# Kernel optimization log

Measured on AMD Instinct MI355X. Metric: run time of the kernel, lower is better.

Reference implementation:

```python
import jax, jax.numpy as jnp
import numpy as np

N, E, IN, H, OUT, L, G = 50000, 800000, 128, 128, 64, 3, 64
NEG_SLOPE = 0.2


def setup_inputs() -> dict:
    key = jax.random.key(0)
    ks = jax.random.split(key, 10)
    x = jax.random.normal(ks[0], (N, IN), dtype=jnp.float32)
    edge_index = jax.random.randint(ks[1], (2, E), 0, N, dtype=jnp.int64)
    batch = jnp.sort(jax.random.randint(ks[2], (N,), 0, G, dtype=jnp.int64))
    s_in = 1.0 / np.sqrt(IN)
    s_h = 1.0 / np.sqrt(H)
    return {
        "x": x,
        "edge_index": edge_index,
        "batch": batch,
        "W0": jax.random.normal(ks[3], (IN, H), dtype=jnp.float32) * s_in,
        "b0": jnp.zeros((H,), dtype=jnp.float32),
        "Wl": jax.random.normal(ks[4], (L, H, H), dtype=jnp.float32) * s_h,
        "a_src": jax.random.normal(ks[5], (L, H), dtype=jnp.float32) * s_h,
        "a_dst": jax.random.normal(ks[6], (L, H), dtype=jnp.float32) * s_h,
        "bl": jnp.zeros((L, H), dtype=jnp.float32),
        "Wf": jax.random.normal(ks[7], (H, OUT), dtype=jnp.float32) * s_h,
        "bf": jnp.zeros((OUT,), dtype=jnp.float32),
    }


def _gat_layer(h, src, dst, n_nodes, W, a_s, a_d, b):
    # GATConv, heads=1: h' = W h; e_ij = leaky_relu(a_s.h'_j + a_d.h'_i)
    hp = h @ W  # [N, H]
    alpha_s = hp @ a_s  # [N]
    alpha_d = hp @ a_d  # [N]
    e = jax.nn.leaky_relu(alpha_s[src] + alpha_d[dst], NEG_SLOPE)  # [E+N]
    # segment softmax over incoming edges of each destination node
    m = jax.ops.segment_max(e, dst, num_segments=n_nodes)
    ex = jnp.exp(e - m[dst])
    denom = jax.ops.segment_sum(ex, dst, num_segments=n_nodes)
    alpha = ex / denom[dst]  # [E+N]
    out = jax.ops.segment_sum(hp[src] * alpha[:, None], dst, num_segments=n_nodes)
    return out + b


def reference(x, edge_index, batch, W0, b0, Wl, a_src, a_dst, bl, Wf, bf):
    n_nodes = x.shape[0]
    loops = jnp.arange(n_nodes, dtype=edge_index.dtype)
    src = jnp.concatenate([edge_index[0], loops])  # add_self_loops=True
    dst = jnp.concatenate([edge_index[1], loops])
    h = x @ W0 + b0  # initial Linear
    n_layers = Wl.shape[0]
    for l in range(n_layers):
        h = _gat_layer(h, src, dst, n_nodes, Wl[l], a_src[l], a_dst[l], bl[l])
        if l < n_layers - 1:
            h = jax.nn.relu(h)  # BasicGNN: act between layers, none after last
    pooled = jax.ops.segment_sum(h, batch, num_segments=G)  # global_add_pool
    return (pooled @ Wf + bf).squeeze()
```

## Files before the change

### kernel.cpp

```cpp
#include <hip/hip_runtime.h>
#include <hip/hip_bf16.h>
#include <math.h>

#define HF 128
#define GCOUNT 64
#define OUTF 64
#define NEG 0.2f
#define CH 2048
#define BCAP 8192

typedef unsigned short u16;
typedef unsigned int   u32;
typedef unsigned char  u8;
typedef short bf16x8 __attribute__((ext_vector_type(8)));
typedef float f32x4  __attribute__((ext_vector_type(4)));
typedef float f32x2  __attribute__((ext_vector_type(2)));

__device__ __forceinline__ u16 f2b(float f) {
    u32 u = __builtin_bit_cast(u32, f);
    u32 r = (u + 0x7FFFu + ((u >> 16) & 1u)) >> 16;
    return (u16)r;
}

__device__ __forceinline__ u8 f2q(float f) {
    return (u8)(__builtin_amdgcn_cvt_pk_fp8_f32(f, f, 0, false) & 0xFF);
}

__global__ void k_pack_init(const float* __restrict__ W0, const float* __restrict__ Wl,
                            u16* __restrict__ P, int* bucketCur, float* pooled) {
    if (blockIdx.x < 32) {
        int m = blockIdx.x >> 3;
        int i = (blockIdx.x & 7) * 256 + threadIdx.x;
        const float* W = (m == 0) ? W0 : Wl + (size_t)(m - 1) * HF * HF;
        u16* Pm = P + (size_t)m * HF * HF;
        int lane = i & 63, kc = (i >> 6) & 3, t = i >> 8;
        int quad = lane >> 4, col = 16 * t + (lane & 15);
        #pragma unroll
        for (int j = 0; j < 8; ++j) {
            int k = kc * 32 + quad * 8 + j;
            Pm[(size_t)i * 8 + j] = f2b(W[k * HF + col]);
        }
    } else if (blockIdx.x == 32) {
        bucketCur[threadIdx.x] = threadIdx.x * BCAP;
    } else {
        pooled[(blockIdx.x - 33) * 256 + threadIdx.x] = 0.f;
    }
}


__device__ __forceinline__ void dev_bpart(int bx, const int* __restrict__ esrc,
                                          const int* __restrict__ edst,
                                          int* __restrict__ bucketCur,
                                          u32* __restrict__ epart, int ne, int ntot) {
    __shared__ int cnt[256];
    __shared__ int base[256];
    int tid = threadIdx.x;
    int t0 = bx * CH, t1 = min(t0 + CH, ntot);
    cnt[tid] = 0;
    __syncthreads();
    int sreg[8], dreg[8];
    #pragma unroll
    for (int it = 0; it < 8; ++it) {
        int t = t0 + tid + it * 256;
        int s = 0, d = -1;
        if (t < t1) {
            if (t < ne) { s = esrc[t]; d = edst[t]; }
            else        { s = t - ne; d = s; }
            atomicAdd(&cnt[d >> 8], 1);
        }
        sreg[it] = s; dreg[it] = d;
    }
    __syncthreads();
    int c = cnt[tid];
    base[tid] = c ? atomicAdd(&bucketCur[tid], c) : 0;
    cnt[tid] = 0;
    __syncthreads();
    #pragma unroll
    for (int it = 0; it < 8; ++it) {
        int d = dreg[it];
        if (d >= 0) {
            int b = d >> 8;
            int pos = base[b] + atomicAdd(&cnt[b], 1);
            epart[pos] = ((u32)sreg[it] << 8) | (u32)(d & 255);
        }
    }
}

__device__ __forceinline__ void dev_bcsr(int bx, const u32* __restrict__ epart,
                                         const int* __restrict__ bucketCur,
                                         int* __restrict__ rowbeg,
                                         int* __restrict__ rowend,
                                         int* __restrict__ colidx, int n) {
    __shared__ int deg[256], offs[256], curs[256], s[256];
    int b = bx, tid = threadIdx.x;
    int e0 = b * BCAP, e1 = bucketCur[b];
    deg[tid] = 0;
    curs[tid] = 0;
    __syncthreads();
    for (int t = e0 + tid; t < e1; t += 256)
        atomicAdd(&deg[epart[t] & 255u], 1);
    __syncthreads();
    int v = deg[tid];
    s[tid] = v;
    __syncthreads();
    int acc = v;
    for (int off = 1; off < 256; off <<= 1) {
        int t = (tid >= off) ? s[tid - off] : 0;
        __syncthreads();
        acc += t;
        s[tid] = acc;
        __syncthreads();
    }
    int excl = acc - v;
    offs[tid] = excl;
    int node = (b << 8) + tid;
    if (node < n) {
        rowbeg[node] = e0 + excl;
        rowend[node] = e0 + excl + v;
    }
    __syncthreads();
    for (int t = e0 + tid; t < e1; t += 256) {
        u32 e = epart[t];
        int l = e & 255u;
        int pos = e0 + offs[l] + atomicAdd(&curs[l], 1);
        colidx[pos] = (int)(e >> 8);
    }
}

template<bool A32, bool Q8>
__device__ __forceinline__ void dev_gemm(int bx, const u16* __restrict__ Ab,
                                         const float* __restrict__ Af,
                                         const u16* __restrict__ Bp,
                                         const float* __restrict__ bias,
                                         const float* __restrict__ a_s,
                                         const float* __restrict__ a_d,
                                         float* __restrict__ as_,
                                         float* __restrict__ ad_,
                                         u16* __restrict__ C,
                                         u8* __restrict__ C8, int M) {
    int lane = threadIdx.x & 63;
    int wave = threadIdx.x >> 6;
    int quad = lane >> 4, l16 = lane & 15;
    int m0 = bx * 64 + wave * 16;
    int arow = m0 + l16;
    bool aval = arow < M;
    const bf16x8* Av = A32 ? nullptr : (const bf16x8*)(Ab + (size_t)arow * HF);
    const bf16x8* Bv = (const bf16x8*)Bp;
    f32x4 acc[8] = {};

    #pragma unroll
    for (int kc = 0; kc < 4; ++kc) {
        bf16x8 a = {};
        if (aval) {
            if constexpr (A32) {
                const float* ap = Af + (size_t)arow * HF + kc * 32 + quad * 8;
                float4 f0 = *(const float4*)ap;
                float4 f1 = *(const float4*)(ap + 4);
                a[0] = (short)f2b(f0.x); a[1] = (short)f2b(f0.y);
                a[2] = (short)f2b(f0.z); a[3] = (short)f2b(f0.w);
                a[4] = (short)f2b(f1.x); a[5] = (short)f2b(f1.y);
                a[6] = (short)f2b(f1.z); a[7] = (short)f2b(f1.w);
            } else {
                a = Av[kc * 4 + quad];
            }
        }
        #pragma unroll
        for (int t = 0; t < 8; ++t)
            acc[t] = __builtin_amdgcn_mfma_f32_16x16x32_bf16(a, Bv[t * 256 + kc * 64 + lane],
                                                             acc[t], 0, 0, 0);
    }

    int orow0 = m0 + quad * 4;
    #pragma unroll
    for (int t = 0; t < 8; ++t) {
        float b4 = bias ? bias[t * 16 + l16] : 0.f;
        #pragma unroll
        for (int r = 0; r < 4; ++r) {
            int orow = orow0 + r;
            if (orow < M) {
                float v = acc[t][r] + b4;
                if constexpr (Q8) C8[(size_t)orow * HF + t * 16 + l16] = f2q(v);
                else              C [(size_t)orow * HF + t * 16 + l16] = f2b(v);
            }
        }
    }

    if (as_) {
        float avs[8], avd[8];
        #pragma unroll
        for (int t = 0; t < 8; ++t) {
            avs[t] = a_s[t * 16 + l16];
            avd[t] = a_d[t * 16 + l16];
        }
        #pragma unroll
        for (int r = 0; r < 4; ++r) {
            float ps = 0.f, pd = 0.f;
            #pragma unroll
            for (int t = 0; t < 8; ++t) {
                ps = fmaf(acc[t][r], avs[t], ps);
                pd = fmaf(acc[t][r], avd[t], pd);
            }
            #pragma unroll
            for (int o = 1; o < 16; o <<= 1) {
                ps += __shfl_xor(ps, o);
                pd += __shfl_xor(pd, o);
            }
            int row = orow0 + r;
            if (l16 == 0 && row < M) { as_[row] = ps; ad_[row] = pd; }
        }
    }
}

__global__ __launch_bounds__(256) void k_gemm0_bpart(const float* __restrict__ x,
                                                     const u16* __restrict__ Wp,
                                                     const float* __restrict__ b0,
                                                     u16* __restrict__ hb, int M, int gemmb,
                                                     const int* __restrict__ esrc,
                                                     const int* __restrict__ edst,
                                                     int* __restrict__ bucketCur,
                                                     u32* __restrict__ epart, int ne, int ntot) {
    if ((int)blockIdx.x < gemmb)
        dev_gemm<true, false>(blockIdx.x, nullptr, x, Wp, b0,
                              nullptr, nullptr, nullptr, nullptr, hb, nullptr, M);
    else
        dev_bpart(blockIdx.x - gemmb, esrc, edst, bucketCur, epart, ne, ntot);
}

__global__ __launch_bounds__(256) void k_gemm1_bcsr(const u16* __restrict__ hb,
                                                    const u16* __restrict__ Bp,
                                                    const float* __restrict__ a_s,
                                                    const float* __restrict__ a_d,
                                                    float* __restrict__ as_,
                                                    float* __restrict__ ad_,
                                                    u8* __restrict__ hp8, int M, int gemmb,
                                                    const u32* __restrict__ epart,
                                                    const int* __restrict__ bucketCur,
                                                    int* __restrict__ rowbeg,
                                                    int* __restrict__ rowend,
                                                    int* __restrict__ colidx, int n) {
    if ((int)blockIdx.x < gemmb)
        dev_gemm<false, true>(blockIdx.x, hb, nullptr, Bp, nullptr,
                              a_s, a_d, as_, ad_, nullptr, hp8, M);
    else
        dev_bcsr(blockIdx.x - gemmb, epart, bucketCur, rowbeg, rowend, colidx, n);
}

__global__ __launch_bounds__(256) void k_gemm_layer(const u16* __restrict__ hb,
                                                    const u16* __restrict__ Bp,
                                                    const float* __restrict__ a_s,
                                                    const float* __restrict__ a_d,
                                                    float* __restrict__ as_,
                                                    float* __restrict__ ad_,
                                                    u8* __restrict__ hp8, int M) {
    dev_gemm<false, true>(blockIdx.x, hb, nullptr, Bp, nullptr,
                          a_s, a_d, as_, ad_, nullptr, hp8, M);
}

template<bool POOL>
__device__ __forceinline__ void dev_agg_item(int it, const int* __restrict__ rowbeg,
                                             const int* __restrict__ rowend,
                                             const int* __restrict__ colidx,
                                             const u8* __restrict__ hp8,
                                             const float* __restrict__ as_,
                                             const float* __restrict__ ad_,
                                             const float* __restrict__ bl,
                                             u16* __restrict__ hout,
                                             int n, int relu,
                                             const int* __restrict__ batch,
                                             float* __restrict__ pooled) {
    int wv = threadIdx.x >> 6;
    int node = it * 4 + wv;
    int lane = threadIdx.x & 63;
    bool valid = node < n;
    int beg = 0, end = 0;
    float adi = 0.f;
    if (valid) { beg = rowbeg[node]; end = rowend[node]; adi = ad_[node]; }
    int deg = end - beg;

    int  srcl = (lane < deg) ? colidx[beg + lane] : 0;
    float el = -1e30f;
    if (lane < deg) {
        float e = as_[srcl] + adi;
        el = e > 0.f ? e : NEG * e;
    }

    float m = el;
    for (int jj = beg + 64 + lane; jj < end; jj += 64) {
        float e = as_[colidx[jj]] + adi;
        e = e > 0.f ? e : NEG * e;
        m = fmaxf(m, e);
    }
    #pragma unroll
    for (int off = 32; off; off >>= 1) m = fmaxf(m, __shfl_xor(m, off));

    float ex = (lane < deg) ? __expf(el - m) : 0.f;
    float ssum = ex;
    for (int jj = beg + 64 + lane; jj < end; jj += 64) {
        float e = as_[colidx[jj]] + adi;
        e = e > 0.f ? e : NEG * e;
        ssum += __expf(e - m);
    }
    #pragma unroll
    for (int off = 32; off; off >>= 1) ssum += __shfl_xor(ssum, off);
    float wl = ex;

    int hl = lane & 31;
    int half = lane >> 5;
    float a0 = 0.f, a1 = 0.f, a2 = 0.f, a3 = 0.f;
    int cnt = deg < 64 ? deg : 64;
    int npair = (cnt + 1) >> 1;

    int p = 0;
    for (; p + 4 <= npair; p += 4) {
        #pragma unroll
        for (int i = 0; i < 4; ++i) {
            int e  = 2 * (p + i) + half;
            int ec = e < cnt ? e : cnt - 1;
            int   s = __shfl(srcl, ec);
            float w = (e < cnt) ? __shfl(wl, ec) : 0.f;
            u32 v = ((const u32*)(hp8 + (size_t)s * HF))[hl];
            f32x2 lo = __builtin_amdgcn_cvt_pk_f32_fp8((int)v, false);
            f32x2 hi = __builtin_amdgcn_cvt_pk_f32_fp8((int)v, true);
            a0 = fmaf(w, lo.x, a0); a1 = fmaf(w, lo.y, a1);
            a2 = fmaf(w, hi.x, a2); a3 = fmaf(w, hi.y, a3);
        }
    }
    for (; p < npair; ++p) {
        int e  = 2 * p + half;
        int ec = e < cnt ? e : cnt - 1;
        int   s = __shfl(srcl, ec);
        float w = (e < cnt) ? __shfl(wl, ec) : 0.f;
        u32 v = ((const u32*)(hp8 + (size_t)s * HF))[hl];
        f32x2 lo = __builtin_amdgcn_cvt_pk_f32_fp8((int)v, false);
        f32x2 hi = __builtin_amdgcn_cvt_pk_f32_fp8((int)v, true);
        a0 = fmaf(w, lo.x, a0); a1 = fmaf(w, lo.y, a1);
        a2 = fmaf(w, hi.x, a2); a3 = fmaf(w, hi.y, a3);
    }
    for (int jj = beg + 64; jj < end; ++jj) {
        int srcn = colidx[jj];
        float e = as_[srcn] + adi;
        e = e > 0.f ? e : NEG * e;
        float w = (half == 0) ? __expf(e - m) : 0.f;
        u32 v = ((const u32*)(hp8 + (size_t)srcn * HF))[hl];
        f32x2 lo = __builtin_amdgcn_cvt_pk_f32_fp8((int)v, false);
        f32x2 hi = __builtin_amdgcn_cvt_pk_f32_fp8((int)v, true);
        a0 = fmaf(w, lo.x, a0); a1 = fmaf(w, lo.y, a1);
        a2 = fmaf(w, hi.x, a2); a3 = fmaf(w, hi.y, a3);
    }

    a0 += __shfl_xor(a0, 32); a1 += __shfl_xor(a1, 32);
    a2 += __shfl_xor(a2, 32); a3 += __shfl_xor(a3, 32);

    if constexpr (!POOL) {
        if (half == 0 && valid) {
            float inv = 1.f / ssum;
            float4 bb = ((const float4*)bl)[hl];
            a0 = fmaf(a0, inv, bb.x); a1 = fmaf(a1, inv, bb.y);
            a2 = fmaf(a2, inv, bb.z); a3 = fmaf(a3, inv, bb.w);
            if (relu) {
                a0 = fmaxf(a0, 0.f); a1 = fmaxf(a1, 0.f);
                a2 = fmaxf(a2, 0.f); a3 = fmaxf(a3, 0.f);
            }
            uint2 o;
            o.x = ((u32)f2b(a1) << 16) | (u32)f2b(a0);
            o.y = ((u32)f2b(a3) << 16) | (u32)f2b(a2);
            ((uint2*)(hout + (size_t)node * HF))[hl] = o;
        }
    } else {
        __shared__ float ptile[4][HF];
        if (half == 0) {
            float o0 = 0.f, o1 = 0.f, o2 = 0.f, o3 = 0.f;
            if (valid) {
                float inv = 1.f / ssum;
                float4 bb = ((const float4*)bl)[hl];
                o0 = fmaf(a0, inv, bb.x); o1 = fmaf(a1, inv, bb.y);
                o2 = fmaf(a2, inv, bb.z); o3 = fmaf(a3, inv, bb.w);
            }
            ptile[wv][hl * 4 + 0] = o0; ptile[wv][hl * 4 + 1] = o1;
            ptile[wv][hl * 4 + 2] = o2; ptile[wv][hl * 4 + 3] = o3;
        }
        __syncthreads();
        int tid = threadIdx.x;
        if (tid < HF) {
            float acc = 0.f;
            int curb = -1;
            #pragma unroll
            for (int s2 = 0; s2 < 4; ++s2) {
                int nd = it * 4 + s2;
                if (nd < n) {
                    int b = batch[nd];
                    if (b != curb) {
                        if (curb >= 0) atomicAdd(&pooled[curb * HF + tid], acc);
                        curb = b;
                        acc = 0.f;
                    }
                    acc += ptile[s2][tid];
                }
            }
            if (curb >= 0) atomicAdd(&pooled[curb * HF + tid], acc);
        }
    }
}

__global__ __launch_bounds__(256) void k_agg(const int* __restrict__ rowbeg,
                                             const int* __restrict__ rowend,
                                             const int* __restrict__ colidx,
                                             const u8* __restrict__ hp8,
                                             const float* __restrict__ as_,
                                             const float* __restrict__ ad_,
                                             const float* __restrict__ bl,
                                             u16* __restrict__ hout,
                                             int n, int relu) {
    dev_agg_item<false>(blockIdx.x, rowbeg, rowend, colidx, hp8, as_, ad_, bl,
                        hout, n, relu, nullptr, nullptr);
}

__global__ __launch_bounds__(256) void k_agg_pool(const int* __restrict__ rowbeg,
                                                  const int* __restrict__ rowend,
                                                  const int* __restrict__ colidx,
                                                  const u8* __restrict__ hp8,
                                                  const float* __restrict__ as_,
                                                  const float* __restrict__ ad_,
                                                  const float* __restrict__ bl,
                                                  int n,
                                                  const int* __restrict__ batch,
                                                  float* __restrict__ pooled) {
    dev_agg_item<true>(blockIdx.x, rowbeg, rowend, colidx, hp8, as_, ad_, bl,
                       nullptr, n, 0, batch, pooled);
}

__global__ void k_final(const float* __restrict__ pooled, const float* __restrict__ Wf,
                        const float* __restrict__ bf, float* __restrict__ out) {
    int g = blockIdx.x, o = threadIdx.x;
    float acc = bf[o];
    #pragma unroll 8
    for (int k = 0; k < HF; ++k) acc = fmaf(pooled[g * HF + k], Wf[k * OUTF + o], acc);
    out[g * OUTF + o] = acc;
}

extern "C" void kernel_launch(void* const* d_in, const int* in_sizes, int n_in,
                              void* d_out, int out_size, void* d_ws, size_t ws_size,
                              hipStream_t stream) {
    const float* x      = (const float*)d_in[0];
    const int*   edge   = (const int*)d_in[1];
    const int*   batch  = (const int*)d_in[2];
    const float* W0     = (const float*)d_in[3];
    const float* b0     = (const float*)d_in[4];
    const float* Wl     = (const float*)d_in[5];
    const float* a_src  = (const float*)d_in[6];
    const float* a_dst  = (const float*)d_in[7];
    const float* bl     = (const float*)d_in[8];
    const float* Wf     = (const float*)d_in[9];
    const float* bf     = (const float*)d_in[10];
    float* out = (float*)d_out;

    const int N  = in_sizes[2];
    const int E  = in_sizes[1] / 2;
    const int Et = E + N;
    const int L  = 3;
    const int NB = (N + 255) >> 8;

    char* ws = (char*)d_ws;
    size_t off = 0;
    auto alloc = [&](size_t bytes) { char* p = ws + off; off += (bytes + 255) & ~(size_t)255; return p; };
    u16*   hb      = (u16*)alloc((size_t)N * HF * 2);
    u8*    hp8     = (u8*)alloc((size_t)N * HF);
    u16*   Wp      = (u16*)alloc((size_t)4 * HF * HF * 2);
    float* as_     = (float*)alloc((size_t)N * 4);
    float* ad_     = (float*)alloc((size_t)N * 4);
    int*   rowbeg  = (int*)alloc((size_t)N * 4);
    int*   rowend  = (int*)alloc((size_t)N * 4);
    int*   colidx  = (int*)alloc((size_t)NB * BCAP * 4);
    u32*   epart   = (u32*)alloc((size_t)NB * BCAP * 4);
    int*   bucketCur = (int*)alloc(256 * 4);
    float* pooled  = (float*)alloc((size_t)GCOUNT * HF * 4);
    (void)ws_size; (void)n_in; (void)out_size;

    const int wb4   = (N + 3) / 4;
    const int gemmb = (N + 63) / 64;
    const int partb = (Et + CH - 1) / CH;

    const int* esrc = edge;
    const int* edst = edge + E;

    k_pack_init<<<65, 256, 0, stream>>>(W0, Wl, Wp, bucketCur, pooled);

    k_gemm0_bpart<<<gemmb + partb, 256, 0, stream>>>(x, Wp, b0, hb, N, gemmb,
                                                     esrc, edst, bucketCur, epart, E, Et);

    k_gemm1_bcsr<<<gemmb + NB, 256, 0, stream>>>(hb, Wp + (size_t)1 * HF * HF,
                                                 a_src, a_dst, as_, ad_, hp8, N, gemmb,
                                                 epart, bucketCur, rowbeg, rowend, colidx, N);

    for (int l = 0; l < L; ++l) {
        if (l > 0)
            k_gemm_layer<<<gemmb, 256, 0, stream>>>(hb, Wp + (size_t)(l + 1) * HF * HF,
                                                    a_src + l * HF, a_dst + l * HF,
                                                    as_, ad_, hp8, N);
        if (l < L - 1)
            k_agg<<<wb4, 256, 0, stream>>>(rowbeg, rowend, colidx, hp8, as_, ad_,
                                           bl + l * HF, hb, N, 1);
        else
            k_agg_pool<<<wb4, 256, 0, stream>>>(rowbeg, rowend, colidx, hp8, as_, ad_,
                                                bl + l * HF, N, batch, pooled);
    }

    k_final<<<GCOUNT, OUTF, 0, stream>>>(pooled, Wf, bf, out);
}
```

Baseline: 266.3 us.

## Software-pipeline fp8 neighbor gathers with 16-lane rows and 8-byte loads

Restructures the aggregation gather so each node row is handled by 16 lanes doing 8-byte fp8 loads, with four edges in flight per group instead of two. Loads for the first edge group are issued before the softmax max/sum reductions, and the following groups are double-buffered so memory latency overlaps with compute. This is meant to hide gather latency and cut the number of load instructions. In exchange it uses more registers (8 accumulators plus 8 u64 buffers) and needs an extra cross-lane reduction step.

```diff
diff --git a/kernel.cpp b/kernel.cpp
--- a/kernel.cpp
+++ b/kernel.cpp
@@ -12,6 +12,7 @@
 typedef unsigned short u16;
 typedef unsigned int   u32;
 typedef unsigned char  u8;
+typedef unsigned long long u64;
 typedef short bf16x8 __attribute__((ext_vector_type(8)));
 typedef float f32x4  __attribute__((ext_vector_type(4)));
 typedef float f32x2  __attribute__((ext_vector_type(2)));
@@ -46,7 +47,6 @@
         pooled[(blockIdx.x - 33) * 256 + threadIdx.x] = 0.f;
     }
 }
-
 
 __device__ __forceinline__ void dev_bpart(int bx, const int* __restrict__ esrc,
                                           const int* __restrict__ edst,
@@ -256,6 +256,46 @@
                           a_s, a_d, as_, ad_, nullptr, hp8, M);
 }
 
+__device__ __forceinline__ void agg_fma(u64 q, float w, float (&acc)[8]) {
+    u32 lo = (u32)q, hi = (u32)(q >> 32);
+    f32x2 p0 = __builtin_amdgcn_cvt_pk_f32_fp8((int)lo, false);
+    f32x2 p1 = __builtin_amdgcn_cvt_pk_f32_fp8((int)lo, true);
+    f32x2 p2 = __builtin_amdgcn_cvt_pk_f32_fp8((int)hi, false);
+    f32x2 p3 = __builtin_amdgcn_cvt_pk_f32_fp8((int)hi, true);
+    acc[0] = fmaf(w, p0.x, acc[0]); acc[1] = fmaf(w, p0.y, acc[1]);
+    acc[2] = fmaf(w, p1.x, acc[2]); acc[3] = fmaf(w, p1.y, acc[3]);
+    acc[4] = fmaf(w, p2.x, acc[4]); acc[5] = fmaf(w, p2.y, acc[5]);
+    acc[6] = fmaf(w, p3.x, acc[6]); acc[7] = fmaf(w, p3.y, acc[7]);
+}
+
+#define AGG_ISSUE(g, q0, q1, q2, q3)                                             \
+    {                                                                            \
+        int e0_ = (g)*16 + 0*4 + sub, e1_ = (g)*16 + 1*4 + sub;                  \
+        int e2_ = (g)*16 + 2*4 + sub, e3_ = (g)*16 + 3*4 + sub;                  \
+        int s0_ = __shfl(srcl, min(e0_, ecmax));                                 \
+        int s1_ = __shfl(srcl, min(e1_, ecmax));                                 \
+        int s2_ = __shfl(srcl, min(e2_, ecmax));                                 \
+        int s3_ = __shfl(srcl, min(e3_, ecmax));                                 \
+        q0 = *(const u64*)(hp8 + (size_t)s0_ * HF + fo);                         \
+        q1 = *(const u64*)(hp8 + (size_t)s1_ * HF + fo);                         \
+        q2 = *(const u64*)(hp8 + (size_t)s2_ * HF + fo);                         \
+        q3 = *(const u64*)(hp8 + (size_t)s3_ * HF + fo);                         \
+    }
+
+#define AGG_CONSUME(g, q0, q1, q2, q3)                                           \
+    {                                                                            \
+        int e0_ = (g)*16 + 0*4 + sub, e1_ = (g)*16 + 1*4 + sub;                  \
+        int e2_ = (g)*16 + 2*4 + sub, e3_ = (g)*16 + 3*4 + sub;                  \
+        float w0_ = __shfl(wl, min(e0_, ecmax));                                 \
+        float w1_ = __shfl(wl, min(e1_, ecmax));                                 \
+        float w2_ = __shfl(wl, min(e2_, ecmax));                                 \
+        float w3_ = __shfl(wl, min(e3_, ecmax));                                 \
+        agg_fma(q0, (e0_ < cnt) ? w0_ : 0.f, acc);                               \
+        agg_fma(q1, (e1_ < cnt) ? w1_ : 0.f, acc);                               \
+        agg_fma(q2, (e2_ < cnt) ? w2_ : 0.f, acc);                               \
+        agg_fma(q3, (e3_ < cnt) ? w3_ : 0.f, acc);                               \
+    }
+
 template<bool POOL>
 __device__ __forceinline__ void dev_agg_item(int it, const int* __restrict__ rowbeg,
                                              const int* __restrict__ rowend,
@@ -271,19 +311,27 @@
     int wv = threadIdx.x >> 6;
     int node = it * 4 + wv;
     int lane = threadIdx.x & 63;
+    int sub = lane >> 4;
+    int fo  = (lane & 15) * 8;
     bool valid = node < n;
     int beg = 0, end = 0;
     float adi = 0.f;
     if (valid) { beg = rowbeg[node]; end = rowend[node]; adi = ad_[node]; }
     int deg = end - beg;
-
-    int  srcl = (lane < deg) ? colidx[beg + lane] : 0;
+    int cnt = deg < 64 ? deg : 64;
+    int ecmax = cnt > 1 ? cnt - 1 : 0;
+
+    int srcl = (lane < deg) ? colidx[beg + lane] : 0;
+
+    float acc[8] = {};
+    u64 qA0, qA1, qA2, qA3, qB0, qB1, qB2, qB3;
+    AGG_ISSUE(0, qA0, qA1, qA2, qA3);
+
     float el = -1e30f;
     if (lane < deg) {
         float e = as_[srcl] + adi;
         el = e > 0.f ? e : NEG * e;
     }
-
     float m = el;
     for (int jj = beg + 64 + lane; jj < end; jj += 64) {
         float e = as_[colidx[jj]] + adi;
@@ -304,85 +352,77 @@
     for (int off = 32; off; off >>= 1) ssum += __shfl_xor(ssum, off);
     float wl = ex;
 
-    int hl = lane & 31;
-    int half = lane >> 5;
-    float a0 = 0.f, a1 = 0.f, a2 = 0.f, a3 = 0.f;
-    int cnt = deg < 64 ? deg : 64;
-    int npair = (cnt + 1) >> 1;
-
-    int p = 0;
-    for (; p + 4 <= npair; p += 4) {
-        #pragma unroll
-        for (int i = 0; i < 4; ++i) {
-            int e  = 2 * (p + i) + half;
-            int ec = e < cnt ? e : cnt - 1;
-            int   s = __shfl(srcl, ec);
-            float w = (e < cnt) ? __shfl(wl, ec) : 0.f;
-            u32 v = ((const u32*)(hp8 + (size_t)s * HF))[hl];
-            f32x2 lo = __builtin_amdgcn_cvt_pk_f32_fp8((int)v, false);
-            f32x2 hi = __builtin_amdgcn_cvt_pk_f32_fp8((int)v, true);
-            a0 = fmaf(w, lo.x, a0); a1 = fmaf(w, lo.y, a1);
-            a2 = fmaf(w, hi.x, a2); a3 = fmaf(w, hi.y, a3);
-        }
-    }
-    for (; p < npair; ++p) {
-        int e  = 2 * p + half;
-        int ec = e < cnt ? e : cnt - 1;
-        int   s = __shfl(srcl, ec);
-        float w = (e < cnt) ? __shfl(wl, ec) : 0.f;
-        u32 v = ((const u32*)(hp8 + (size_t)s * HF))[hl];
-        f32x2 lo = __builtin_amdgcn_cvt_pk_f32_fp8((int)v, false);
-        f32x2 hi = __builtin_amdgcn_cvt_pk_f32_fp8((int)v, true);
-        a0 = fmaf(w, lo.x, a0); a1 = fmaf(w, lo.y, a1);
-        a2 = fmaf(w, hi.x, a2); a3 = fmaf(w, hi.y, a3);
-    }
-    for (int jj = beg + 64; jj < end; ++jj) {
-        int srcn = colidx[jj];
-        float e = as_[srcn] + adi;
-        e = e > 0.f ? e : NEG * e;
-        float w = (half == 0) ? __expf(e - m) : 0.f;
-        u32 v = ((const u32*)(hp8 + (size_t)srcn * HF))[hl];
-        f32x2 lo = __builtin_amdgcn_cvt_pk_f32_fp8((int)v, false);
-        f32x2 hi = __builtin_amdgcn_cvt_pk_f32_fp8((int)v, true);
-        a0 = fmaf(w, lo.x, a0); a1 = fmaf(w, lo.y, a1);
-        a2 = fmaf(w, hi.x, a2); a3 = fmaf(w, hi.y, a3);
-    }
-
-    a0 += __shfl_xor(a0, 32); a1 += __shfl_xor(a1, 32);
-    a2 += __shfl_xor(a2, 32); a3 += __shfl_xor(a3, 32);
+    bool g1 = cnt > 16, g2 = cnt > 32, g3 = cnt > 48;
+    if (g1) AGG_ISSUE(1, qB0, qB1, qB2, qB3);
+    AGG_CONSUME(0, qA0, qA1, qA2, qA3);
+    if (g1) {
+        if (g2) AGG_ISSUE(2, qA0, qA1, qA2, qA3);
+        AGG_CONSUME(1, qB0, qB1, qB2, qB3);
+        if (g2) {
+            if (g3) AGG_ISSUE(3, qB0, qB1, qB2, qB3);
+            AGG_CONSUME(2, qA0, qA1, qA2, qA3);
+            if (g3) AGG_CONSUME(3, qB0, qB1, qB2, qB3);
+        }
+    }
+
+    for (int jj = beg + 64; jj < end; jj += 4) {
+        int e = jj + sub;
+        bool v = e < end;
+        int s = colidx[v ? e : end - 1];
+        float w = 0.f;
+        if (v) {
+            float x = as_[s] + adi;
+            x = x > 0.f ? x : NEG * x;
+            w = __expf(x - m);
+        }
+        u64 q = *(const u64*)(hp8 + (size_t)s * HF + fo);
+        agg_fma(q, w, acc);
+    }
+
+    #pragma unroll
+    for (int k = 0; k < 8; ++k) {
+        acc[k] += __shfl_xor(acc[k], 16);
+        acc[k] += __shfl_xor(acc[k], 32);
+    }
 
     if constexpr (!POOL) {
-        if (half == 0 && valid) {
+        if (lane < 16 && valid) {
             float inv = 1.f / ssum;
-            float4 bb = ((const float4*)bl)[hl];
-            a0 = fmaf(a0, inv, bb.x); a1 = fmaf(a1, inv, bb.y);
-            a2 = fmaf(a2, inv, bb.z); a3 = fmaf(a3, inv, bb.w);
+            float4 bb0 = ((const float4*)bl)[lane * 2];
+            float4 bb1 = ((const float4*)bl)[lane * 2 + 1];
+            float o0 = fmaf(acc[0], inv, bb0.x), o1 = fmaf(acc[1], inv, bb0.y);
+            float o2 = fmaf(acc[2], inv, bb0.z), o3 = fmaf(acc[3], inv, bb0.w);
+            float o4 = fmaf(acc[4], inv, bb1.x), o5 = fmaf(acc[5], inv, bb1.y);
+            float o6 = fmaf(acc[6], inv, bb1.z), o7 = fmaf(acc[7], inv, bb1.w);
             if (relu) {
-                a0 = fmaxf(a0, 0.f); a1 = fmaxf(a1, 0.f);
-                a2 = fmaxf(a2, 0.f); a3 = fmaxf(a3, 0.f);
-            }
-            uint2 o;
-            o.x = ((u32)f2b(a1) << 16) | (u32)f2b(a0);
-            o.y = ((u32)f2b(a3) << 16) | (u32)f2b(a2);
-            ((uint2*)(hout + (size_t)node * HF))[hl] = o;
+                o0 = fmaxf(o0, 0.f); o1 = fmaxf(o1, 0.f);
+                o2 = fmaxf(o2, 0.f); o3 = fmaxf(o3, 0.f);
+                o4 = fmaxf(o4, 0.f); o5 = fmaxf(o5, 0.f);
+                o6 = fmaxf(o6, 0.f); o7 = fmaxf(o7, 0.f);
+            }
+            uint4 o;
+            o.x = ((u32)f2b(o1) << 16) | (u32)f2b(o0);
+            o.y = ((u32)f2b(o3) << 16) | (u32)f2b(o2);
+            o.z = ((u32)f2b(o5) << 16) | (u32)f2b(o4);
+            o.w = ((u32)f2b(o7) << 16) | (u32)f2b(o6);
+            ((uint4*)(hout + (size_t)node * HF))[lane] = o;
         }
     } else {
         __shared__ float ptile[4][HF];
-        if (half == 0) {
-            float o0 = 0.f, o1 = 0.f, o2 = 0.f, o3 = 0.f;
-            if (valid) {
-                float inv = 1.f / ssum;
-                float4 bb = ((const float4*)bl)[hl];
-                o0 = fmaf(a0, inv, bb.x); o1 = fmaf(a1, inv, bb.y);
-                o2 = fmaf(a2, inv, bb.z); o3 = fmaf(a3, inv, bb.w);
-            }
-            ptile[wv][hl * 4 + 0] = o0; ptile[wv][hl * 4 + 1] = o1;
-            ptile[wv][hl * 4 + 2] = o2; ptile[wv][hl * 4 + 3] = o3;
+        if (lane < 16) {
+            float inv = valid ? 1.f / ssum : 0.f;
+            float4 bb0 = ((const float4*)bl)[lane * 2];
+            float4 bb1 = ((const float4*)bl)[lane * 2 + 1];
+            #pragma unroll
+            for (int k = 0; k < 8; ++k) {
+                float b = (k < 4) ? ((const float*)&bb0)[k] : ((const float*)&bb1)[k - 4];
+                ptile[wv][lane * 8 + k] = valid ? fmaf(acc[k], inv, b) : 0.f;
+            }
         }
         __syncthreads();
         int tid = threadIdx.x;
         if (tid < HF) {
-            float acc = 0.f;
+            float a = 0.f;
             int curb = -1;
             #pragma unroll
             for (int s2 = 0; s2 < 4; ++s2) {
@@ -390,14 +430,14 @@
                 if (nd < n) {
                     int b = batch[nd];
                     if (b != curb) {
-                        if (curb >= 0) atomicAdd(&pooled[curb * HF + tid], acc);
+                        if (curb >= 0) atomicAdd(&pooled[curb * HF + tid], a);
                         curb = b;
-                        acc = 0.f;
+                        a = 0.f;
                     }
-                    acc += ptile[s2][tid];
+                    a += ptile[s2][tid];
                 }
             }
-            if (curb >= 0) atomicAdd(&pooled[curb * HF + tid], acc);
+            if (curb >= 0) atomicAdd(&pooled[curb * HF + tid], a);
         }
     }
 }
```

After: 272.8 us. 2.4% more time.
